# Kernel optimization log

Hardware: AMD Instinct MI355X
Metric: run time of the kernel (lower is better)

## Reference

```python
import jax, jax.numpy as jnp
import numpy as np

N, NFEAT, NHID = 10000, 128, 64


def _gc(x, adj, W, b):
    # GraphConvolution: adj @ (x @ W) + b
    return adj @ (x @ W) + b


def _fwd(x, adj, Wg0, bg0, Wg1, bg1, Wt0, bt0, Wt1, bt1,
         W000, b000, W001, b001, W100, b100, W101, b101,
         Wo0, bo0, Wo1, bo1, Wpp, bpp, Wpp2, bpp2, a, t):
    H = Wg0.shape[1]
    # outcome GCN stack (n_in=2), dropout is eval no-op
    rep_o = jax.nn.relu(_gc(x, adj, Wg0, bg0))
    rep_o = jax.nn.relu(_gc(rep_o, adj, Wg1, bg1))
    # treatment GCN stack
    rep_t = jax.nn.relu(_gc(x, adj, Wt0, bt0))
    rep_t = jax.nn.relu(_gc(rep_t, adj, Wt1, bt1))

    rep_cat = jnp.concatenate([rep_o, rep_t], axis=1)  # [N, 2H]
    # edge score(i,j) = [rep_cat_i ; rep_cat_j] @ a  =  s_src_i + s_dst_j
    s_src = rep_cat @ a[:2 * H, 0]   # [N]
    s_dst = rep_cat @ a[2 * H:, 0]   # [N]
    scores = s_src[:, None] + s_dst[None, :]          # [N, N]
    # only nonzero adj entries get a score; rest remain 0 (index_put into zeros)
    att = jnp.where(adj != 0, scores, jnp.zeros((), scores.dtype))
    att = jax.nn.softmax(att, axis=1)                 # full dense row softmax

    rep_out = att @ rep_t + rep_o                     # [N, H]

    treatment = jax.nn.sigmoid((rep_t @ Wpp + bpp) @ Wpp2 + bpp2)  # [N, 2]

    rep0 = rep_out
    rep1 = rep_out
    y00 = jax.nn.relu(rep0 @ W000 + b000)
    y10 = jax.nn.relu(rep1 @ W100 + b100)
    y00 = jax.nn.relu(y00 @ W001 + b001)
    y10 = jax.nn.relu(y10 @ W101 + b101)
    y0 = (y00 @ Wo0 + bo0).reshape(-1)
    y1 = (y10 @ Wo1 + bo1).reshape(-1)
    y = jnp.where(t > 0, y1, y0)
    return (y, rep_out, treatment)


def setup_inputs() -> dict:
    key = jax.random.key(0)
    ks = jax.random.split(key, 32)
    H = NHID
    x = jax.random.normal(ks[0], (N, NFEAT), dtype=jnp.float32)
    u = jax.random.uniform(ks[1], (N, N), dtype=jnp.float32)
    adj = jnp.where(u < 0.002, u, jnp.zeros((), jnp.float32))
    t = jax.random.randint(ks[2], (N,), 0, 2, dtype=jnp.int32)

    def lin(k, fi, fo):
        s = 1.0 / np.sqrt(fi)
        kw, kb = jax.random.split(k)
        return (jax.random.uniform(kw, (fi, fo), jnp.float32, -s, s),
                jax.random.uniform(kb, (fo,), jnp.float32, -s, s))

    Wg0, bg0 = lin(ks[3], NFEAT, H)
    Wg1, bg1 = lin(ks[4], H, H)
    Wt0, bt0 = lin(ks[5], NFEAT, H)
    Wt1, bt1 = lin(ks[6], H, H)
    W000, b000 = lin(ks[7], H, H)
    W001, b001 = lin(ks[8], H, H)
    W100, b100 = lin(ks[9], H, H)
    W101, b101 = lin(ks[10], H, H)
    Wo0, bo0 = lin(ks[11], H, 1)
    Wo1, bo1 = lin(ks[12], H, 1)
    Wpp, bpp = lin(ks[13], H, H)
    Wpp2, bpp2 = lin(ks[14], H, 2)
    # torch init is xavier with gain=0 (all zeros); use small random for a
    # meaningful correctness baseline
    a = jax.random.normal(ks[15], (4 * H, 1), dtype=jnp.float32) * 0.1
    return dict(x=x, adj=adj, t=t,
                Wg0=Wg0, bg0=bg0, Wg1=Wg1, bg1=bg1,
                Wt0=Wt0, bt0=bt0, Wt1=Wt1, bt1=bt1,
                W000=W000, b000=b000, W001=W001, b001=b001,
                W100=W100, b100=b100, W101=W101, b101=b101,
                Wo0=Wo0, bo0=bo0, Wo1=Wo1, bo1=bo1,
                Wpp=Wpp, bpp=bpp, Wpp2=Wpp2, bpp2=bpp2, a=a)


def reference(x, adj, t, Wg0, bg0, Wg1, bg1, Wt0, bt0, Wt1, bt1,
              W000, b000, W001, b001, W100, b100, W101, b101,
              Wo0, bo0, Wo1, bo1, Wpp, bpp, Wpp2, bpp2, a):
    return _fwd(x, adj, Wg0, bg0, Wg1, bg1, Wt0, bt0, Wt1, bt1,
                W000, b000, W001, b001, W100, b100, W101, b101,
                Wo0, bo0, Wo1, bo1, Wpp, bpp, Wpp2, bpp2, a, t)
```

## Files before the change

kernel.cpp:

```cpp
#include <hip/hip_runtime.h>
#include <hip/hip_bf16.h>

#define N_NODES 10000
#define ROW4    2500
#define CAP     64
#define SPAR_BLOCKS 2500
#define TOTAL_K1    3750

typedef float fx4 __attribute__((ext_vector_type(4)));

#define OFF_CNT     0
#define OFF_COLSUM  10000
#define OFF_SSRC    10064
#define OFF_SDST    20064
#define OFF_PAIRS   30064
#define OFF_B1      1310064
#define OFF_B2      1950064
#define OFF_B3      2590064
#define OFF_B4      3230064

__device__ __forceinline__ float wave_sum(float v) {
    #pragma unroll
    for (int off = 32; off >= 1; off >>= 1) v += __shfl_xor(v, off, 64);
    return v;
}
__device__ __forceinline__ float wave_max(float v) {
    #pragma unroll
    for (int off = 32; off >= 1; off >>= 1) v = fmaxf(v, __shfl_xor(v, off, 64));
    return v;
}

__global__ void k1_fused(const fx4* __restrict__ adj4, const float* __restrict__ x,
                         const float* __restrict__ Wg0, const float* __restrict__ Wt0,
                         int* __restrict__ cnt, float2* __restrict__ pairs,
                         float* __restrict__ colsum,
                         float* __restrict__ P, float* __restrict__ Q) {
    __shared__ float xs[8 * 128];
    int tid = threadIdx.x;
    if (blockIdx.x < SPAR_BLOCKS) {
        int lane = tid & 63, w = tid >> 6;
        int row = (SPAR_BLOCKS - 1 - (int)blockIdx.x) * 4 + w;
        if (blockIdx.x == 0 && tid < 64) colsum[tid] = 0.0f;
        const fx4* rp = adj4 + (size_t)row * ROW4;
        size_t base = (size_t)row * CAP;
        int count = 0;
        for (int it = 0; it < 40; it += 8) {
            fx4 v[8];
            #pragma unroll
            for (int j = 0; j < 8; ++j) {
                int idx = (it + j) * 64 + lane;
                v[j] = (fx4){0.f, 0.f, 0.f, 0.f};
                if (idx < ROW4) v[j] = __builtin_nontemporal_load(rp + idx);
            }
            #pragma unroll
            for (int j = 0; j < 8; ++j) {
                int idx = (it + j) * 64 + lane;
                float vv[4] = {v[j].x, v[j].y, v[j].z, v[j].w};
                bool any = (vv[0] != 0.f) | (vv[1] != 0.f) | (vv[2] != 0.f) | (vv[3] != 0.f);
                if (__ballot(any)) {
                    #pragma unroll
                    for (int l = 0; l < 4; ++l) {
                        unsigned long long b = __ballot(vv[l] != 0.f);
                        if (b) {
                            int pre = __popcll(b & ((1ull << lane) - 1ull));
                            if (vv[l] != 0.f) {
                                int pos = count + pre;
                                if (pos < CAP)
                                    pairs[base + pos] =
                                        make_float2(__int_as_float(idx * 4 + l), vv[l]);
                            }
                            count += (int)__popcll(b);
                        }
                    }
                }
            }
        }
        if (lane == 0) cnt[row] = min(count, CAP);
    } else {
        int row0 = (blockIdx.x - SPAR_BLOCKS) * 8;
        ((float4*)xs)[tid] = ((const float4*)(x + (size_t)row0 * 128))[tid];
        __syncthreads();
        int sub = tid >> 6, f = tid & 63;
        #pragma unroll
        for (int g = 0; g < 2; ++g) {
            const float* xr = xs + (g * 4 + sub) * 128;
            float aP = 0.0f, aQ = 0.0f;
            #pragma unroll 8
            for (int k = 0; k < 128; k += 4) {
                float4 xv = *(const float4*)(xr + k);
                aP += xv.x * Wg0[(k + 0) * 64 + f] + xv.y * Wg0[(k + 1) * 64 + f]
                    + xv.z * Wg0[(k + 2) * 64 + f] + xv.w * Wg0[(k + 3) * 64 + f];
                aQ += xv.x * Wt0[(k + 0) * 64 + f] + xv.y * Wt0[(k + 1) * 64 + f]
                    + xv.z * Wt0[(k + 2) * 64 + f] + xv.w * Wt0[(k + 3) * 64 + f];
            }
            P[(size_t)(row0 + g * 4 + sub) * 64 + f] = aP;
            Q[(size_t)(row0 + g * 4 + sub) * 64 + f] = aQ;
        }
    }
}

__global__ void k2_agg_gemm(const int* __restrict__ cnt, const float2* __restrict__ pairs,
                            const float* __restrict__ P, const float* __restrict__ Q,
                            const float* __restrict__ bg0, const float* __restrict__ bt0,
                            const float* __restrict__ Wg1, const float* __restrict__ Wt1,
                            float* __restrict__ P2, float* __restrict__ Q2) {
    __shared__ float ra[8 * 64], rb[8 * 64];
    int tid = threadIdx.x, row0 = blockIdx.x * 8, sub = tid >> 6, f = tid & 63;
    float bo = bg0[f], bt = bt0[f];
    #pragma unroll
    for (int g = 0; g < 2; ++g) {
        int lr = g * 4 + sub, row = row0 + lr;
        int c = min(cnt[row], CAP);
        float2 pr = make_float2(0.f, 0.f);
        if (f < c) pr = pairs[(size_t)row * CAP + f];
        int c_l = __float_as_int(pr.x); float v_l = pr.y;
        float a0 = 0.f, a1 = 0.f, b0 = 0.f, b1 = 0.f;
        for (int p = 0; p < c; p += 8) {
            #pragma unroll
            for (int j = 0; j < 8; j += 2) {
                float vv0 = __shfl(v_l, p + j, 64);     int cc0 = __shfl(c_l, p + j, 64);
                float vv1 = __shfl(v_l, p + j + 1, 64); int cc1 = __shfl(c_l, p + j + 1, 64);
                a0 += vv0 * P[(size_t)cc0 * 64 + f];
                b0 += vv0 * Q[(size_t)cc0 * 64 + f];
                a1 += vv1 * P[(size_t)cc1 * 64 + f];
                b1 += vv1 * Q[(size_t)cc1 * 64 + f];
            }
        }
        ra[lr * 64 + f] = fmaxf(a0 + a1 + bo, 0.0f);
        rb[lr * 64 + f] = fmaxf(b0 + b1 + bt, 0.0f);
    }
    __syncthreads();
    #pragma unroll
    for (int g = 0; g < 2; ++g) {
        int lr = g * 4 + sub, row = row0 + lr;
        const float* rra = ra + lr * 64;
        const float* rrb = rb + lr * 64;
        float aA = 0.f, aB = 0.f;
        #pragma unroll 8
        for (int k = 0; k < 64; k += 4) {
            float4 va = *(const float4*)(rra + k);
            float4 vb = *(const float4*)(rrb + k);
            aA += va.x * Wg1[(k + 0) * 64 + f] + va.y * Wg1[(k + 1) * 64 + f]
                + va.z * Wg1[(k + 2) * 64 + f] + va.w * Wg1[(k + 3) * 64 + f];
            aB += vb.x * Wt1[(k + 0) * 64 + f] + vb.y * Wt1[(k + 1) * 64 + f]
                + vb.z * Wt1[(k + 2) * 64 + f] + vb.w * Wt1[(k + 3) * 64 + f];
        }
        P2[(size_t)row * 64 + f] = aA;
        Q2[(size_t)row * 64 + f] = aB;
    }
}

__global__ void k3_agg_score(const int* __restrict__ cnt, const float2* __restrict__ pairs,
                             const float* __restrict__ P2, const float* __restrict__ Q2,
                             const float* __restrict__ bg1, const float* __restrict__ bt1,
                             const float* __restrict__ a,
                             const float* __restrict__ Wpp, const float* __restrict__ bpp,
                             const float* __restrict__ Wpp2, const float* __restrict__ bpp2,
                             float* __restrict__ rep_o, float* __restrict__ rep_t,
                             float* __restrict__ s_src, float* __restrict__ s_dst,
                             float* __restrict__ colsum, float* __restrict__ out_trt) {
    __shared__ float rts[8 * 64];
    int tid = threadIdx.x, row0 = blockIdx.x * 8, sub = tid >> 6, f = tid & 63;
    float bo = bg1[f], bt = bt1[f];
    float a0c = a[f], a1c = a[64 + f], a2c = a[128 + f], a3c = a[192 + f];
    #pragma unroll
    for (int g = 0; g < 2; ++g) {
        int lr = g * 4 + sub, row = row0 + lr;
        int c = min(cnt[row], CAP);
        float2 pr = make_float2(0.f, 0.f);
        if (f < c) pr = pairs[(size_t)row * CAP + f];
        int c_l = __float_as_int(pr.x); float v_l = pr.y;
        float a0 = 0.f, a1 = 0.f, b0 = 0.f, b1 = 0.f;
        for (int p = 0; p < c; p += 8) {
            #pragma unroll
            for (int j = 0; j < 8; j += 2) {
                float vv0 = __shfl(v_l, p + j, 64);     int cc0 = __shfl(c_l, p + j, 64);
                float vv1 = __shfl(v_l, p + j + 1, 64); int cc1 = __shfl(c_l, p + j + 1, 64);
                a0 += vv0 * P2[(size_t)cc0 * 64 + f];
                b0 += vv0 * Q2[(size_t)cc0 * 64 + f];
                a1 += vv1 * P2[(size_t)cc1 * 64 + f];
                b1 += vv1 * Q2[(size_t)cc1 * 64 + f];
            }
        }
        float vo = fmaxf(a0 + a1 + bo, 0.0f);
        float vt = fmaxf(b0 + b1 + bt, 0.0f);
        rep_o[(size_t)row * 64 + f] = vo;
        rep_t[(size_t)row * 64 + f] = vt;
        rts[lr * 64 + f] = vt;
        float ps = wave_sum(vo * a0c + vt * a1c);
        float pd = wave_sum(vo * a2c + vt * a3c);
        if (f == 0) { s_src[row] = ps; s_dst[row] = pd; }
    }
    __syncthreads();
    if (sub == 0) {
        float cs = 0.0f;
        #pragma unroll
        for (int lr = 0; lr < 8; ++lr) cs += rts[lr * 64 + f];
        atomicAdd(&colsum[f], cs);
    }
    float bp = bpp[f], w20 = Wpp2[f * 2 + 0], w21 = Wpp2[f * 2 + 1];
    #pragma unroll
    for (int g = 0; g < 2; ++g) {
        int lr = g * 4 + sub, row = row0 + lr;
        const float* rr = rts + lr * 64;
        float u = bp;
        #pragma unroll 8
        for (int k = 0; k < 64; k += 4) {
            float4 rv = *(const float4*)(rr + k);
            u += rv.x * Wpp[(k + 0) * 64 + f] + rv.y * Wpp[(k + 1) * 64 + f]
               + rv.z * Wpp[(k + 2) * 64 + f] + rv.w * Wpp[(k + 3) * 64 + f];
        }
        float p0 = wave_sum(u * w20);
        float p1 = wave_sum(u * w21);
        if (f == 0) {
            out_trt[(size_t)row * 2 + 0] = 1.0f / (1.0f + expf(-(p0 + bpp2[0])));
            out_trt[(size_t)row * 2 + 1] = 1.0f / (1.0f + expf(-(p1 + bpp2[1])));
        }
    }
}

__global__ void k4_attn_heads(const int* __restrict__ cnt, const float2* __restrict__ pairs,
                              const float* __restrict__ s_src, const float* __restrict__ s_dst,
                              const float* __restrict__ colsum,
                              const float* __restrict__ rep_o, const float* __restrict__ rep_t,
                              const float* __restrict__ W000, const float* __restrict__ b000,
                              const float* __restrict__ W001, const float* __restrict__ b001,
                              const float* __restrict__ W100, const float* __restrict__ b100,
                              const float* __restrict__ W101, const float* __restrict__ b101,
                              const float* __restrict__ Wo0, const float* __restrict__ bo0,
                              const float* __restrict__ Wo1, const float* __restrict__ bo1,
                              const int* __restrict__ t,
                              float* __restrict__ out_y, float* __restrict__ out_rep) {
    __shared__ float reps[8 * 64], u0s[8 * 64], u1s[8 * 64];
    int tid = threadIdx.x, row0 = blockIdx.x * 8, sub = tid >> 6, f = tid & 63;
    float csf = colsum[f];
    #pragma unroll
    for (int g = 0; g < 2; ++g) {
        int lr = g * 4 + sub, row = row0 + lr;
        int c = min(cnt[row], CAP);
        float ssrc = s_src[row];
        int   col_l = (f < c) ? __float_as_int(pairs[(size_t)row * CAP + f].x) : 0;
        float s_l   = (f < c) ? ssrc + s_dst[col_l] : -1e30f;
        float m = fmaxf(wave_max(s_l), 0.0f);
        float e_l = (f < c) ? expf(s_l - m) : 0.0f;
        float em = expf(-m);
        float Z = wave_sum(e_l) + (float)(N_NODES - c) * em;
        float g_l = (f < c) ? (e_l - em) : 0.0f;
        float a0 = 0.f, a1 = 0.f, a2 = 0.f, a3 = 0.f;
        for (int p = 0; p < c; p += 8) {
            #pragma unroll
            for (int j = 0; j < 8; j += 4) {
                float g0 = __shfl(g_l, p + j + 0, 64); int c0 = __shfl(col_l, p + j + 0, 64);
                float g1 = __shfl(g_l, p + j + 1, 64); int c1 = __shfl(col_l, p + j + 1, 64);
                float g2 = __shfl(g_l, p + j + 2, 64); int c2 = __shfl(col_l, p + j + 2, 64);
                float g3 = __shfl(g_l, p + j + 3, 64); int c3 = __shfl(col_l, p + j + 3, 64);
                a0 += g0 * rep_t[(size_t)c0 * 64 + f];
                a1 += g1 * rep_t[(size_t)c1 * 64 + f];
                a2 += g2 * rep_t[(size_t)c2 * 64 + f];
                a3 += g3 * rep_t[(size_t)c3 * 64 + f];
            }
        }
        float outv = ((a0 + a1 + a2 + a3) + em * csf) / Z + rep_o[(size_t)row * 64 + f];
        out_rep[(size_t)row * 64 + f] = outv;
        reps[lr * 64 + f] = outv;
    }
    __syncthreads();
    float bA = b000[f], bB = b100[f];
    #pragma unroll
    for (int g = 0; g < 2; ++g) {
        int lr = g * 4 + sub;
        const float* rr = reps + lr * 64;
        float u0 = bA, u1 = bB;
        #pragma unroll 8
        for (int k = 0; k < 64; k += 4) {
            float4 rv = *(const float4*)(rr + k);
            u0 += rv.x * W000[(k + 0) * 64 + f] + rv.y * W000[(k + 1) * 64 + f]
                + rv.z * W000[(k + 2) * 64 + f] + rv.w * W000[(k + 3) * 64 + f];
            u1 += rv.x * W100[(k + 0) * 64 + f] + rv.y * W100[(k + 1) * 64 + f]
                + rv.z * W100[(k + 2) * 64 + f] + rv.w * W100[(k + 3) * 64 + f];
        }
        u0s[lr * 64 + f] = fmaxf(u0, 0.0f);
        u1s[lr * 64 + f] = fmaxf(u1, 0.0f);
    }
    __syncthreads();
    float bC = b001[f], bD = b101[f], wo0 = Wo0[f], wo1 = Wo1[f];
    #pragma unroll
    for (int g = 0; g < 2; ++g) {
        int lr = g * 4 + sub, row = row0 + lr;
        const float* r0 = u0s + lr * 64;
        const float* r1 = u1s + lr * 64;
        float v0 = bC, v1 = bD;
        #pragma unroll 8
        for (int k = 0; k < 64; k += 4) {
            float4 q0 = *(const float4*)(r0 + k);
            float4 q1 = *(const float4*)(r1 + k);
            v0 += q0.x * W001[(k + 0) * 64 + f] + q0.y * W001[(k + 1) * 64 + f]
                + q0.z * W001[(k + 2) * 64 + f] + q0.w * W001[(k + 3) * 64 + f];
            v1 += q1.x * W101[(k + 0) * 64 + f] + q1.y * W101[(k + 1) * 64 + f]
                + q1.z * W101[(k + 2) * 64 + f] + q1.w * W101[(k + 3) * 64 + f];
        }
        float y0 = wave_sum(fmaxf(v0, 0.0f) * wo0);
        float y1 = wave_sum(fmaxf(v1, 0.0f) * wo1);
        if (f == 0)
            out_y[row] = (t[row] > 0) ? (y1 + bo1[0]) : (y0 + bo0[0]);
    }
}


extern "C" void kernel_launch(void* const* d_in, const int* in_sizes, int n_in,
                              void* d_out, int out_size, void* d_ws, size_t ws_size,
                              hipStream_t stream) {
    const float* x    = (const float*)d_in[0];
    const float* adj  = (const float*)d_in[1];
    const int*   t    = (const int*)d_in[2];
    const float* Wg0  = (const float*)d_in[3];
    const float* bg0  = (const float*)d_in[4];
    const float* Wg1  = (const float*)d_in[5];
    const float* bg1  = (const float*)d_in[6];
    const float* Wt0  = (const float*)d_in[7];
    const float* bt0  = (const float*)d_in[8];
    const float* Wt1  = (const float*)d_in[9];
    const float* bt1  = (const float*)d_in[10];
    const float* W000 = (const float*)d_in[11];
    const float* b000 = (const float*)d_in[12];
    const float* W001 = (const float*)d_in[13];
    const float* b001 = (const float*)d_in[14];
    const float* W100 = (const float*)d_in[15];
    const float* b100 = (const float*)d_in[16];
    const float* W101 = (const float*)d_in[17];
    const float* b101 = (const float*)d_in[18];
    const float* Wo0  = (const float*)d_in[19];
    const float* bo0  = (const float*)d_in[20];
    const float* Wo1  = (const float*)d_in[21];
    const float* bo1  = (const float*)d_in[22];
    const float* Wpp  = (const float*)d_in[23];
    const float* bpp  = (const float*)d_in[24];
    const float* Wpp2 = (const float*)d_in[25];
    const float* bpp2 = (const float*)d_in[26];
    const float* a    = (const float*)d_in[27];

    float* ws = (float*)d_ws;
    int*    cnt    = (int*)(ws + OFF_CNT);
    float*  colsum = ws + OFF_COLSUM;
    float*  s_src  = ws + OFF_SSRC;
    float*  s_dst  = ws + OFF_SDST;
    float2* pairs  = (float2*)(ws + OFF_PAIRS);
    float*  B1     = ws + OFF_B1;
    float*  B2     = ws + OFF_B2;
    float*  B3     = ws + OFF_B3;
    float*  B4     = ws + OFF_B4;

    float* out_y   = (float*)d_out;
    float* out_rep = (float*)d_out + N_NODES;
    float* out_trt = (float*)d_out + N_NODES + N_NODES * 64;

    k1_fused<<<TOTAL_K1, 256, 0, stream>>>((const fx4*)adj, x, Wg0, Wt0,
                                           cnt, pairs, colsum, B1, B2);
    k2_agg_gemm<<<1250, 256, 0, stream>>>(cnt, pairs, B1, B2, bg0, bt0, Wg1, Wt1, B3, B4);
    k3_agg_score<<<1250, 256, 0, stream>>>(cnt, pairs, B3, B4, bg1, bt1, a,
                                           Wpp, bpp, Wpp2, bpp2,
                                           B1, B2, s_src, s_dst, colsum, out_trt);
    k4_attn_heads<<<1250, 256, 0, stream>>>(cnt, pairs, s_src, s_dst, colsum, B1, B2,
                                            W000, b000, W001, b001,
                                            W100, b100, W101, b101,
                                            Wo0, bo0, Wo1, bo1, t, out_y, out_rep);
}
```

Measured before the change: 652.8 us.

## Fuse four kernels into one persistent kernel with grid barriers

Replaces the four stage kernels with a single cooperative-style kernel of 1250 blocks that uses atomic-counter grid barriers between stages. The adjacency scan now covers two rows per wave inside the same blocks that do the x@W GEMM. The goal is to remove inter-kernel launch gaps and tail effects. In exchange it depends on all blocks being co-resident, checked via an occupancy query with a fallback to the old path, and it adds barrier spin costs plus a memset per call.

```diff
diff --git a/kernel.cpp b/kernel.cpp
--- a/kernel.cpp
+++ b/kernel.cpp
@@ -4,6 +4,8 @@
 #define N_NODES 10000
 #define ROW4    2500
 #define CAP     64
+#define NBLK    1250
+
 #define SPAR_BLOCKS 2500
 #define TOTAL_K1    3750
 
@@ -18,6 +20,7 @@
 #define OFF_B2      1950064
 #define OFF_B3      2590064
 #define OFF_B4      3230064
+#define OFF_BAR     3870064
 
 __device__ __forceinline__ float wave_sum(float v) {
     #pragma unroll
@@ -28,6 +31,300 @@
     #pragma unroll
     for (int off = 32; off >= 1; off >>= 1) v = fmaxf(v, __shfl_xor(v, off, 64));
     return v;
+}
+
+__device__ __forceinline__ void gsync(int* __restrict__ bar, int idx) {
+    __syncthreads();
+    if (threadIdx.x == 0) {
+        __threadfence();
+        int prev = __hip_atomic_fetch_add(&bar[idx], 1, __ATOMIC_ACQ_REL,
+                                          __HIP_MEMORY_SCOPE_AGENT);
+        if (prev < NBLK - 1) {
+            while (__hip_atomic_load(&bar[idx], __ATOMIC_ACQUIRE,
+                                     __HIP_MEMORY_SCOPE_AGENT) < NBLK)
+                __builtin_amdgcn_s_sleep(2);
+        }
+        __threadfence();
+    }
+    __syncthreads();
+}
+
+__global__ void __launch_bounds__(256, 5)
+mega(const fx4* __restrict__ adj4, const float* __restrict__ x,
+     const float* __restrict__ Wg0, const float* __restrict__ bg0,
+     const float* __restrict__ Wg1, const float* __restrict__ bg1,
+     const float* __restrict__ Wt0, const float* __restrict__ bt0,
+     const float* __restrict__ Wt1, const float* __restrict__ bt1,
+     const float* __restrict__ a,
+     const float* __restrict__ Wpp, const float* __restrict__ bpp,
+     const float* __restrict__ Wpp2, const float* __restrict__ bpp2,
+     const float* __restrict__ W000, const float* __restrict__ b000,
+     const float* __restrict__ W001, const float* __restrict__ b001,
+     const float* __restrict__ W100, const float* __restrict__ b100,
+     const float* __restrict__ W101, const float* __restrict__ b101,
+     const float* __restrict__ Wo0, const float* __restrict__ bo0,
+     const float* __restrict__ Wo1, const float* __restrict__ bo1,
+     const int* __restrict__ t,
+     int* __restrict__ cnt, float2* __restrict__ pairs,
+     float* __restrict__ colsum, float* __restrict__ s_src, float* __restrict__ s_dst,
+     float* __restrict__ B1, float* __restrict__ B2,
+     float* __restrict__ B3, float* __restrict__ B4,
+     int* __restrict__ bar,
+     float* __restrict__ out_y, float* __restrict__ out_rep, float* __restrict__ out_trt) {
+    __shared__ __align__(16) float smem[3 * 8 * 64];
+    int tid = threadIdx.x;
+    int sub = tid >> 6, f = tid & 63;
+    int row0 = blockIdx.x * 8;
+
+    {
+        int lane = tid & 63, w = tid >> 6;
+        int wid = (int)blockIdx.x * 4 + w;
+        if (blockIdx.x == 0 && tid < 64) colsum[tid] = 0.0f;
+        #pragma unroll
+        for (int g = 0; g < 2; ++g) {
+            int row = (N_NODES - 1) - (wid * 2 + g);
+            const fx4* rp = adj4 + (size_t)row * ROW4;
+            size_t base = (size_t)row * CAP;
+            int count = 0;
+            for (int it = 0; it < 40; it += 8) {
+                fx4 v[8];
+                #pragma unroll
+                for (int j = 0; j < 8; ++j) {
+                    int idx = (it + j) * 64 + lane;
+                    v[j] = (fx4){0.f, 0.f, 0.f, 0.f};
+                    if (idx < ROW4) v[j] = __builtin_nontemporal_load(rp + idx);
+                }
+                #pragma unroll
+                for (int j = 0; j < 8; ++j) {
+                    int idx = (it + j) * 64 + lane;
+                    float vv[4] = {v[j].x, v[j].y, v[j].z, v[j].w};
+                    bool any = (vv[0] != 0.f) | (vv[1] != 0.f) | (vv[2] != 0.f) | (vv[3] != 0.f);
+                    if (__ballot(any)) {
+                        #pragma unroll
+                        for (int l = 0; l < 4; ++l) {
+                            unsigned long long b = __ballot(vv[l] != 0.f);
+                            if (b) {
+                                int pre = __popcll(b & ((1ull << lane) - 1ull));
+                                if (vv[l] != 0.f) {
+                                    int pos = count + pre;
+                                    if (pos < CAP)
+                                        pairs[base + pos] =
+                                            make_float2(__int_as_float(idx * 4 + l), vv[l]);
+                                }
+                                count += (int)__popcll(b);
+                            }
+                        }
+                    }
+                }
+            }
+            if (lane == 0) cnt[row] = min(count, CAP);
+        }
+        float* xs = smem;
+        ((float4*)xs)[tid] = ((const float4*)(x + (size_t)row0 * 128))[tid];
+        __syncthreads();
+        #pragma unroll
+        for (int g = 0; g < 2; ++g) {
+            const float* xr = xs + (g * 4 + sub) * 128;
+            float aP = 0.0f, aQ = 0.0f;
+            #pragma unroll 8
+            for (int k = 0; k < 128; k += 4) {
+                float4 xv = *(const float4*)(xr + k);
+                aP += xv.x * Wg0[(k + 0) * 64 + f] + xv.y * Wg0[(k + 1) * 64 + f]
+                    + xv.z * Wg0[(k + 2) * 64 + f] + xv.w * Wg0[(k + 3) * 64 + f];
+                aQ += xv.x * Wt0[(k + 0) * 64 + f] + xv.y * Wt0[(k + 1) * 64 + f]
+                    + xv.z * Wt0[(k + 2) * 64 + f] + xv.w * Wt0[(k + 3) * 64 + f];
+            }
+            B1[(size_t)(row0 + g * 4 + sub) * 64 + f] = aP;
+            B2[(size_t)(row0 + g * 4 + sub) * 64 + f] = aQ;
+        }
+    }
+    gsync(bar, 0);
+
+    {
+        float* ra = smem;
+        float* rb = smem + 512;
+        float bo = bg0[f], bt = bt0[f];
+        #pragma unroll
+        for (int g = 0; g < 2; ++g) {
+            int lr = g * 4 + sub, row = row0 + lr;
+            int c = min(cnt[row], CAP);
+            float2 pr = make_float2(0.f, 0.f);
+            if (f < c) pr = pairs[(size_t)row * CAP + f];
+            int c_l = __float_as_int(pr.x); float v_l = pr.y;
+            float a0 = 0.f, a1 = 0.f, b0 = 0.f, b1 = 0.f;
+            for (int p = 0; p < c; p += 8) {
+                #pragma unroll
+                for (int j = 0; j < 8; j += 2) {
+                    float vv0 = __shfl(v_l, p + j, 64);     int cc0 = __shfl(c_l, p + j, 64);
+                    float vv1 = __shfl(v_l, p + j + 1, 64); int cc1 = __shfl(c_l, p + j + 1, 64);
+                    a0 += vv0 * B1[(size_t)cc0 * 64 + f];
+                    b0 += vv0 * B2[(size_t)cc0 * 64 + f];
+                    a1 += vv1 * B1[(size_t)cc1 * 64 + f];
+                    b1 += vv1 * B2[(size_t)cc1 * 64 + f];
+                }
+            }
+            ra[lr * 64 + f] = fmaxf(a0 + a1 + bo, 0.0f);
+            rb[lr * 64 + f] = fmaxf(b0 + b1 + bt, 0.0f);
+        }
+        __syncthreads();
+        #pragma unroll
+        for (int g = 0; g < 2; ++g) {
+            int lr = g * 4 + sub, row = row0 + lr;
+            const float* rra = ra + lr * 64;
+            const float* rrb = rb + lr * 64;
+            float aA = 0.f, aB = 0.f;
+            #pragma unroll 8
+            for (int k = 0; k < 64; k += 4) {
+                float4 va = *(const float4*)(rra + k);
+                float4 vb = *(const float4*)(rrb + k);
+                aA += va.x * Wg1[(k + 0) * 64 + f] + va.y * Wg1[(k + 1) * 64 + f]
+                    + va.z * Wg1[(k + 2) * 64 + f] + va.w * Wg1[(k + 3) * 64 + f];
+                aB += vb.x * Wt1[(k + 0) * 64 + f] + vb.y * Wt1[(k + 1) * 64 + f]
+                    + vb.z * Wt1[(k + 2) * 64 + f] + vb.w * Wt1[(k + 3) * 64 + f];
+            }
+            B3[(size_t)row * 64 + f] = aA;
+            B4[(size_t)row * 64 + f] = aB;
+        }
+    }
+    gsync(bar, 1);
+
+    {
+        float* rts = smem;
+        float bo = bg1[f], bt = bt1[f];
+        float a0c = a[f], a1c = a[64 + f], a2c = a[128 + f], a3c = a[192 + f];
+        #pragma unroll
+        for (int g = 0; g < 2; ++g) {
+            int lr = g * 4 + sub, row = row0 + lr;
+            int c = min(cnt[row], CAP);
+            float2 pr = make_float2(0.f, 0.f);
+            if (f < c) pr = pairs[(size_t)row * CAP + f];
+            int c_l = __float_as_int(pr.x); float v_l = pr.y;
+            float a0 = 0.f, a1 = 0.f, b0 = 0.f, b1 = 0.f;
+            for (int p = 0; p < c; p += 8) {
+                #pragma unroll
+                for (int j = 0; j < 8; j += 2) {
+                    float vv0 = __shfl(v_l, p + j, 64);     int cc0 = __shfl(c_l, p + j, 64);
+                    float vv1 = __shfl(v_l, p + j + 1, 64); int cc1 = __shfl(c_l, p + j + 1, 64);
+                    a0 += vv0 * B3[(size_t)cc0 * 64 + f];
+                    b0 += vv0 * B4[(size_t)cc0 * 64 + f];
+                    a1 += vv1 * B3[(size_t)cc1 * 64 + f];
+                    b1 += vv1 * B4[(size_t)cc1 * 64 + f];
+                }
+            }
+            float vo = fmaxf(a0 + a1 + bo, 0.0f);
+            float vt = fmaxf(b0 + b1 + bt, 0.0f);
+            B1[(size_t)row * 64 + f] = vo;
+            B2[(size_t)row * 64 + f] = vt;
+            rts[lr * 64 + f] = vt;
+            float ps = wave_sum(vo * a0c + vt * a1c);
+            float pd = wave_sum(vo * a2c + vt * a3c);
+            if (f == 0) { s_src[row] = ps; s_dst[row] = pd; }
+        }
+        __syncthreads();
+        if (sub == 0) {
+            float cs = 0.0f;
+            #pragma unroll
+            for (int lr = 0; lr < 8; ++lr) cs += rts[lr * 64 + f];
+            atomicAdd(&colsum[f], cs);
+        }
+        float bp = bpp[f], w20 = Wpp2[f * 2 + 0], w21 = Wpp2[f * 2 + 1];
+        #pragma unroll
+        for (int g = 0; g < 2; ++g) {
+            int lr = g * 4 + sub, row = row0 + lr;
+            const float* rr = rts + lr * 64;
+            float u = bp;
+            #pragma unroll 8
+            for (int k = 0; k < 64; k += 4) {
+                float4 rv = *(const float4*)(rr + k);
+                u += rv.x * Wpp[(k + 0) * 64 + f] + rv.y * Wpp[(k + 1) * 64 + f]
+                   + rv.z * Wpp[(k + 2) * 64 + f] + rv.w * Wpp[(k + 3) * 64 + f];
+            }
+            float p0 = wave_sum(u * w20);
+            float p1 = wave_sum(u * w21);
+            if (f == 0) {
+                out_trt[(size_t)row * 2 + 0] = 1.0f / (1.0f + expf(-(p0 + bpp2[0])));
+                out_trt[(size_t)row * 2 + 1] = 1.0f / (1.0f + expf(-(p1 + bpp2[1])));
+            }
+        }
+    }
+    gsync(bar, 2);
+
+    {
+        float* reps = smem;
+        float* u0s  = smem + 512;
+        float* u1s  = smem + 1024;
+        float csf = colsum[f];
+        #pragma unroll
+        for (int g = 0; g < 2; ++g) {
+            int lr = g * 4 + sub, row = row0 + lr;
+            int c = min(cnt[row], CAP);
+            float ssrc = s_src[row];
+            int   col_l = (f < c) ? __float_as_int(pairs[(size_t)row * CAP + f].x) : 0;
+            float s_l   = (f < c) ? ssrc + s_dst[col_l] : -1e30f;
+            float m = fmaxf(wave_max(s_l), 0.0f);
+            float e_l = (f < c) ? expf(s_l - m) : 0.0f;
+            float em = expf(-m);
+            float Z = wave_sum(e_l) + (float)(N_NODES - c) * em;
+            float g_l = (f < c) ? (e_l - em) : 0.0f;
+            float a0 = 0.f, a1 = 0.f, a2 = 0.f, a3 = 0.f;
+            for (int p = 0; p < c; p += 8) {
+                #pragma unroll
+                for (int j = 0; j < 8; j += 4) {
+                    float g0 = __shfl(g_l, p + j + 0, 64); int c0 = __shfl(col_l, p + j + 0, 64);
+                    float g1 = __shfl(g_l, p + j + 1, 64); int c1 = __shfl(col_l, p + j + 1, 64);
+                    float g2 = __shfl(g_l, p + j + 2, 64); int c2 = __shfl(col_l, p + j + 2, 64);
+                    float g3 = __shfl(g_l, p + j + 3, 64); int c3 = __shfl(col_l, p + j + 3, 64);
+                    a0 += g0 * B2[(size_t)c0 * 64 + f];
+                    a1 += g1 * B2[(size_t)c1 * 64 + f];
+                    a2 += g2 * B2[(size_t)c2 * 64 + f];
+                    a3 += g3 * B2[(size_t)c3 * 64 + f];
+                }
+            }
+            float outv = ((a0 + a1 + a2 + a3) + em * csf) / Z + B1[(size_t)row * 64 + f];
+            out_rep[(size_t)row * 64 + f] = outv;
+            reps[lr * 64 + f] = outv;
+        }
+        __syncthreads();
+        float bA = b000[f], bB = b100[f];
+        #pragma unroll
+        for (int g = 0; g < 2; ++g) {
+            int lr = g * 4 + sub;
+            const float* rr = reps + lr * 64;
+            float u0 = bA, u1 = bB;
+            #pragma unroll 8
+            for (int k = 0; k < 64; k += 4) {
+                float4 rv = *(const float4*)(rr + k);
+                u0 += rv.x * W000[(k + 0) * 64 + f] + rv.y * W000[(k + 1) * 64 + f]
+                    + rv.z * W000[(k + 2) * 64 + f] + rv.w * W000[(k + 3) * 64 + f];
+                u1 += rv.x * W100[(k + 0) * 64 + f] + rv.y * W100[(k + 1) * 64 + f]
+                    + rv.z * W100[(k + 2) * 64 + f] + rv.w * W100[(k + 3) * 64 + f];
+            }
+            u0s[lr * 64 + f] = fmaxf(u0, 0.0f);
+            u1s[lr * 64 + f] = fmaxf(u1, 0.0f);
+        }
+        __syncthreads();
+        float bC = b001[f], bD = b101[f], wo0 = Wo0[f], wo1 = Wo1[f];
+        #pragma unroll
+        for (int g = 0; g < 2; ++g) {
+            int lr = g * 4 + sub, row = row0 + lr;
+            const float* r0 = u0s + lr * 64;
+            const float* r1 = u1s + lr * 64;
+            float v0 = bC, v1 = bD;
+            #pragma unroll 8
+            for (int k = 0; k < 64; k += 4) {
+                float4 q0 = *(const float4*)(r0 + k);
+                float4 q1 = *(const float4*)(r1 + k);
+                v0 += q0.x * W001[(k + 0) * 64 + f] + q0.y * W001[(k + 1) * 64 + f]
+                    + q0.z * W001[(k + 2) * 64 + f] + q0.w * W001[(k + 3) * 64 + f];
+                v1 += q1.x * W101[(k + 0) * 64 + f] + q1.y * W101[(k + 1) * 64 + f]
+                    + q1.z * W101[(k + 2) * 64 + f] + q1.w * W101[(k + 3) * 64 + f];
+            }
+            float y0 = wave_sum(fmaxf(v0, 0.0f) * wo0);
+            float y1 = wave_sum(fmaxf(v1, 0.0f) * wo1);
+            if (f == 0)
+                out_y[row] = (t[row] > 0) ? (y1 + bo1[0]) : (y0 + bo0[0]);
+        }
+    }
 }
 
 __global__ void k1_fused(const fx4* __restrict__ adj4, const float* __restrict__ x,
@@ -349,19 +646,41 @@
     float*  B2     = ws + OFF_B2;
     float*  B3     = ws + OFF_B3;
     float*  B4     = ws + OFF_B4;
+    int*    bar    = (int*)(ws + OFF_BAR);
 
     float* out_y   = (float*)d_out;
     float* out_rep = (float*)d_out + N_NODES;
     float* out_trt = (float*)d_out + N_NODES + N_NODES * 64;
 
-    k1_fused<<<TOTAL_K1, 256, 0, stream>>>((const fx4*)adj, x, Wg0, Wt0,
-                                           cnt, pairs, colsum, B1, B2);
-    k2_agg_gemm<<<1250, 256, 0, stream>>>(cnt, pairs, B1, B2, bg0, bt0, Wg1, Wt1, B3, B4);
-    k3_agg_score<<<1250, 256, 0, stream>>>(cnt, pairs, B3, B4, bg1, bt1, a,
-                                           Wpp, bpp, Wpp2, bpp2,
-                                           B1, B2, s_src, s_dst, colsum, out_trt);
-    k4_attn_heads<<<1250, 256, 0, stream>>>(cnt, pairs, s_src, s_dst, colsum, B1, B2,
-                                            W000, b000, W001, b001,
-                                            W100, b100, W101, b101,
-                                            Wo0, bo0, Wo1, bo1, t, out_y, out_rep);
-}
+    static int s_cap = -1;
+    if (s_cap < 0) {
+        int nb = 0, ncu = 0, dev = 0;
+        (void)hipGetDevice(&dev);
+        if (hipOccupancyMaxActiveBlocksPerMultiprocessor(
+                &nb, reinterpret_cast<const void*>(mega), 256, 0) != hipSuccess) nb = 0;
+        if (hipDeviceGetAttribute(&ncu, hipDeviceAttributeMultiprocessorCount, dev)
+                != hipSuccess) ncu = 0;
+        s_cap = nb * ncu;
+    }
+
+    if (s_cap >= NBLK && ws_size >= (size_t)(OFF_BAR + 4) * sizeof(float)) {
+        hipMemsetAsync(bar, 0, 4 * sizeof(int), stream);
+        mega<<<NBLK, 256, 0, stream>>>(
+            (const fx4*)adj, x, Wg0, bg0, Wg1, bg1, Wt0, bt0, Wt1, bt1, a,
+            Wpp, bpp, Wpp2, bpp2, W000, b000, W001, b001, W100, b100, W101, b101,
+            Wo0, bo0, Wo1, bo1, t,
+            cnt, pairs, colsum, s_src, s_dst, B1, B2, B3, B4, bar,
+            out_y, out_rep, out_trt);
+    } else {
+        k1_fused<<<TOTAL_K1, 256, 0, stream>>>((const fx4*)adj, x, Wg0, Wt0,
+                                               cnt, pairs, colsum, B1, B2);
+        k2_agg_gemm<<<1250, 256, 0, stream>>>(cnt, pairs, B1, B2, bg0, bt0, Wg1, Wt1, B3, B4);
+        k3_agg_score<<<1250, 256, 0, stream>>>(cnt, pairs, B3, B4, bg1, bt1, a,
+                                               Wpp, bpp, Wpp2, bpp2,
+                                               B1, B2, s_src, s_dst, colsum, out_trt);
+        k4_attn_heads<<<1250, 256, 0, stream>>>(cnt, pairs, s_src, s_dst, colsum, B1, B2,
+                                                W000, b000, W001, b001,
+                                                W100, b100, W101, b101,
+                                                Wo0, bo0, Wo1, bo1, t, out_y, out_rep);
+    }
+}
```

New measurement: 651.3 us. No clear change (-0.2%).
